# Kernel optimization log

Hardware: AMD Instinct MI355X
Metric: run time of the kernel (lower is better)

The kernel has to match this reference:

```python
import jax, jax.numpy as jnp
import numpy as np

EMB = 1024
HEADS = 16
EPS = 1e-6


def setup_inputs() -> dict:
    key = jax.random.key(0)
    ks = jax.random.split(key, 11)
    B, T = 4, 2048
    s = 0.02
    inp = {
        "x": jax.random.normal(ks[0], (B, T, EMB), dtype=jnp.float32),
        "Wq": jax.random.normal(ks[1], (EMB, EMB), dtype=jnp.float32) * s,
        "bq": jnp.zeros((EMB,), dtype=jnp.float32),
        "Wk": jax.random.normal(ks[2], (EMB, EMB), dtype=jnp.float32) * s,
        "bk": jnp.zeros((EMB,), dtype=jnp.float32),
        "Wv": jax.random.normal(ks[3], (EMB, EMB), dtype=jnp.float32) * s,
        "bv": jnp.zeros((EMB,), dtype=jnp.float32),
        "Wp": jax.random.normal(ks[4], (EMB, EMB), dtype=jnp.float32) * s,
        "bp": jnp.zeros((EMB,), dtype=jnp.float32),
        "gamma": jnp.ones((EMB,), dtype=jnp.float32),
        "beta": jnp.zeros((EMB,), dtype=jnp.float32),
    }
    return inp


def reference(x, Wq, bq, Wk, bk, Wv, bv, Wp, bp, gamma, beta):
    B, T, E = x.shape
    H = HEADS
    hd = E // H
    residual = x
    # torch Linear: y = x @ W.T + b
    q = (jnp.einsum('bte,fe->btf', x, Wq) + bq).reshape(B, T, H, hd).transpose(0, 2, 1, 3)
    k = (jnp.einsum('bte,fe->btf', x, Wk) + bk).reshape(B, T, H, hd).transpose(0, 2, 1, 3)
    v = (jnp.einsum('bte,fe->btf', x, Wv) + bv).reshape(B, T, H, hd).transpose(0, 2, 1, 3)
    # NOTE: original scales by 1/sqrt(T), not 1/sqrt(head_size)
    scale = 1.0 / jnp.sqrt(jnp.asarray(T, dtype=x.dtype))
    att = jnp.einsum('bhqd,bhkd->bhqk', q, k) * scale
    causal = jnp.tril(jnp.ones((T, T), dtype=bool))
    att = jnp.where(causal, att, -jnp.inf)
    att = jax.nn.softmax(att, axis=-1)
    out = jnp.einsum('bhqk,bhkd->bhqd', att, v)
    out = out.transpose(0, 2, 1, 3).reshape(B, T, E)
    # residual added BEFORE projection (as in original)
    out = jnp.einsum('bte,fe->btf', out + residual, Wp) + bp
    # LayerNorm(eps=1e-6)
    mu = jnp.mean(out, axis=-1, keepdims=True)
    var = jnp.mean(jnp.square(out - mu), axis=-1, keepdims=True)
    out = (out - mu) / jnp.sqrt(var + EPS) * gamma + beta
    return out
```

## Files before the change

### kernel.cpp

```cpp
#include <hip/hip_runtime.h>
#include <hip/hip_bf16.h>
#include <cstdint>
#include <cstdio>

#define EMB    1024
#define HEADS  16
#define HD     64
#define TSEQ   2048
#define NBATCH 4
#define BT     (NBATCH*TSEQ)
#define QKVN   3072
#define QKLD   2048

#define CSCALE (1.4426950408889634f * 0.022097086912079608f)

typedef __hip_bfloat16 bf16;
typedef __attribute__((ext_vector_type(8))) short short8;
typedef __attribute__((ext_vector_type(4))) short short4v;
typedef __attribute__((ext_vector_type(4))) float f32x4;

#define MFMA32(A,B,C) __builtin_amdgcn_mfma_f32_16x16x32_bf16(A,B,C,0,0,0)
#if __has_builtin(__builtin_amdgcn_mfma_f32_16x16x16_bf16)
#define MFMA16(A,B,C) __builtin_amdgcn_mfma_f32_16x16x16_bf16(A,B,C,0,0,0)
#else
#define MFMA16(A,B,C) __builtin_amdgcn_mfma_f32_16x16x16bf16_1k(A,B,C,0,0,0)
#endif

#if __has_builtin(__builtin_amdgcn_exp2f)
#define EXP2(x) __builtin_amdgcn_exp2f(x)
#else
#define EXP2(x) exp2f(x)
#endif

template<bool B> struct BoolC { static constexpr bool value = B; };

__device__ __forceinline__ void gload_lds16(const void* g, void* l) {
  __builtin_amdgcn_global_load_lds(
      (const __attribute__((address_space(1))) void*)g,
      (__attribute__((address_space(3))) void*)l,
      16, 0, 0);
}

__device__ __forceinline__ unsigned pkbf(float a, float b) {
  unsigned ua = __builtin_bit_cast(unsigned, a) + 0x8000u;
  unsigned ub = __builtin_bit_cast(unsigned, b) + 0x8000u;
  return __builtin_amdgcn_perm(ub, ua, 0x07060302u);
}

#define BARRIER() do { asm volatile("" ::: "memory"); \
                       __builtin_amdgcn_s_barrier(); \
                       asm volatile("" ::: "memory"); } while (0)
#define BAR_VM(N) do { asm volatile("s_waitcnt vmcnt(" #N ")" ::: "memory"); \
                       __builtin_amdgcn_s_barrier(); \
                       asm volatile("" ::: "memory"); } while (0)

__global__ void fused_cast(const float* __restrict__ x, const float* __restrict__ Wq,
                           const float* __restrict__ Wk, const float* __restrict__ Wv,
                           const float* __restrict__ Wp, const float* __restrict__ bq,
                           const float* __restrict__ bk, const float* __restrict__ bv,
                           bf16* __restrict__ xb, bf16* __restrict__ wqkv,
                           bf16* __restrict__ wpb, float* __restrict__ biasqkv) {
  const int blk = blockIdx.x;
  const int i = threadIdx.x * 4;
  if (blk >= 12288) {
    const int wsel = blk - 12288;
    const float* bsrc = wsel == 0 ? bq : (wsel == 1 ? bk : bv);
    float4 bv4 = *(const float4*)(bsrc + i);
    if (wsel == 0) { bv4.x *= CSCALE; bv4.y *= CSCALE; bv4.z *= CSCALE; bv4.w *= CSCALE; }
    *(float4*)(biasqkv + wsel * 1024 + i) = bv4;
    return;
  }
  const float* src; bf16* dst; float sc = 1.0f;
  if (blk < 8192)       { src = x  + (size_t)blk * 1024;           dst = xb   + (size_t)blk * 1024; }
  else if (blk < 9216)  { src = Wq + (size_t)(blk - 8192) * 1024;  dst = wqkv + (size_t)(blk - 8192) * 1024; sc = CSCALE; }
  else if (blk < 10240) { src = Wk + (size_t)(blk - 9216) * 1024;  dst = wqkv + ((size_t)1 << 20) + (size_t)(blk - 9216) * 1024; }
  else if (blk < 11264) { src = Wv + (size_t)(blk - 10240) * 1024; dst = wqkv + ((size_t)2 << 20) + (size_t)(blk - 10240) * 1024; }
  else                  { src = Wp + (size_t)(blk - 11264) * 1024; dst = wpb  + (size_t)(blk - 11264) * 1024; }
  float4 v = *(const float4*)(src + i);
  union { short4v v; bf16 b[4]; } u;
  u.b[0] = __float2bfloat16(v.x * sc); u.b[1] = __float2bfloat16(v.y * sc);
  u.b[2] = __float2bfloat16(v.z * sc); u.b[3] = __float2bfloat16(v.w * sc);
  *(short4v*)(dst + i) = u.v;
}

#define PHASE_MFMA(MI0, NJ0) do { \
  __builtin_amdgcn_s_setprio(1); \
  _Pragma("unroll") \
  for (int m2 = 0; m2 < 4; ++m2) { \
    _Pragma("unroll") \
    for (int n2 = 0; n2 < 2; ++n2) { \
      acc[(MI0)+m2][(NJ0)+n2] = MFMA32(af[m2][0], bfr[(NJ0)+n2][0], acc[(MI0)+m2][(NJ0)+n2]); \
      acc[(MI0)+m2][(NJ0)+n2] = MFMA32(af[m2][1], bfr[(NJ0)+n2][1], acc[(MI0)+m2][(NJ0)+n2]); \
    } \
  } \
  __builtin_amdgcn_s_setprio(0); \
} while (0)

#define TILE(T, P) { \
  const int kn = ((T) + 1) * 64; \
  const bool st = (T) < 15; \
  const char* aB = rdA + (P) * 32768; \
  const char* bB = rdB + (P) * 32768; \
  char* sA = ldsA + ((P) ^ 1) * 32768 + wbase; \
  char* sB = ldsB + ((P) ^ 1) * 32768 + wbase; \
   \
  _Pragma("unroll") \
  for (int m2 = 0; m2 < 4; ++m2) { \
    af[m2][0] = *(const short8*)(aB + m2 * 2048 + cs0); \
    af[m2][1] = *(const short8*)(aB + m2 * 2048 + cs1); \
  } \
  _Pragma("unroll") \
  for (int n2 = 0; n2 < 2; ++n2) { \
    bfr[n2][0] = *(const short8*)(bB + n2 * 2048 + cs0); \
    bfr[n2][1] = *(const short8*)(bB + n2 * 2048 + cs1); \
  } \
  if (st) { gload_lds16(gB + kn,          sB);         \
            gload_lds16(gB + 131072 + kn, sB + 16384); } \
  BARRIER(); \
  PHASE_MFMA(0, 0); \
  BARRIER(); \
   \
  _Pragma("unroll") \
  for (int n2 = 2; n2 < 4; ++n2) { \
    bfr[n2][0] = *(const short8*)(bB + n2 * 2048 + cs0); \
    bfr[n2][1] = *(const short8*)(bB + n2 * 2048 + cs1); \
  } \
  if (st) { gload_lds16(gA + kn,          sA);         \
            gload_lds16(gA + 131072 + kn, sA + 16384); } \
  BARRIER(); \
  PHASE_MFMA(0, 2); \
  if (st) { BAR_VM(4); } else { BAR_VM(0); } \
   \
  _Pragma("unroll") \
  for (int m2 = 0; m2 < 4; ++m2) { \
    af[m2][0] = *(const short8*)(aB + (4 + m2) * 2048 + cs0); \
    af[m2][1] = *(const short8*)(aB + (4 + m2) * 2048 + cs1); \
  } \
  if (st) { gload_lds16(gB + 65536 + kn,  sB + 8192);  \
            gload_lds16(gB + 196608 + kn, sB + 24576); } \
  BARRIER(); \
  PHASE_MFMA(4, 2); \
  BARRIER(); \
   \
  if (st) { gload_lds16(gA + 65536 + kn,  sA + 8192);  \
            gload_lds16(gA + 196608 + kn, sA + 24576); } \
  PHASE_MFMA(4, 0); \
  if (st) { BAR_VM(2); } \
}

__global__ __launch_bounds__(512, 2) void gemm_qkv8(
    const bf16* __restrict__ A, const bf16* __restrict__ B,
    const float* __restrict__ bias, bf16* __restrict__ qkout,
    bf16* __restrict__ vt) {
  __shared__ short smem[65536];
  const int tid = threadIdx.x;
  const int l = tid & 63, w = tid >> 6;
  const int r = l & 15, qd = l >> 4;
  const int wm = w >> 2, wn = w & 3;

  const int f0 = blockIdx.x;
  const int sid = (f0 & 7) * 48 + (f0 >> 3);
  const int m0 = (sid / 12) * 256;
  const int n0 = (sid % 12) * 256;

  const int rowA = tid >> 3;
  const int chk = (tid & 7) ^ (rowA & 7);
  const bf16* gA = A + (size_t)(m0 + rowA) * 1024 + chk * 8;
  const bf16* gB = B + (size_t)(n0 + rowA) * 1024 + chk * 8;
  char* ldsA = (char*)smem;
  char* ldsB = (char*)smem + 65536;
  const int wbase = w * 1024;

  const char* rdA = (const char*)smem + wm * 16384 + r * 128;
  const char* rdB = (const char*)smem + 65536 + (wn >> 1) * 16384 +
                    ((wn & 1) * 64 + r) * 128;
  const int cs0 = (qd ^ (r & 7)) * 16;
  const int cs1 = ((4 + qd) ^ (r & 7)) * 16;

  f32x4 acc[8][4];
#pragma unroll
  for (int i = 0; i < 8; ++i)
#pragma unroll
    for (int j = 0; j < 4; ++j) acc[i][j] = (f32x4){0.f, 0.f, 0.f, 0.f};
  short8 af[4][2], bfr[4][2];

  {
    char* sA = ldsA + wbase;
    char* sB = ldsB + wbase;
    gload_lds16(gB,          sB);
    gload_lds16(gB + 131072, sB + 16384);
    gload_lds16(gA,          sA);
    gload_lds16(gA + 131072, sA + 16384);
    gload_lds16(gB + 65536,  sB + 8192);
    gload_lds16(gB + 196608, sB + 24576);
    gload_lds16(gA + 65536,  sA + 8192);
    gload_lds16(gA + 196608, sA + 24576);
    BAR_VM(2);
  }

#pragma unroll 1
  for (int tt = 0; tt < 8; ++tt) {
    TILE(tt * 2, 0)
    TILE(tt * 2 + 1, 1)
  }

  if (n0 < 2048) {
#pragma unroll
    for (int nt = 0; nt < 4; ++nt) {
      const int col = n0 + wn * 64 + nt * 16 + r;
      const float bv = bias[col];
#pragma unroll
      for (int mi = 0; mi < 8; ++mi) {
#pragma unroll
        for (int reg = 0; reg < 4; ++reg) {
          const int row = m0 + wm * 128 + mi * 16 + qd * 4 + reg;
          qkout[(size_t)row * QKLD + col] = __float2bfloat16(acc[mi][nt][reg] + bv);
        }
      }
    }
  } else {
    char* img = (char*)smem;
#pragma unroll
    for (int nt = 0; nt < 4; ++nt) {
      const int c_local = wn * 64 + nt * 16 + r;
      const float bv = bias[n0 + c_local];
      const int d7 = c_local & 7;
#pragma unroll
      for (int mi = 0; mi < 8; ++mi) {
        const int tbase = wm * 128 + mi * 16 + qd * 4;
        const int chunk = tbase >> 6;
        const int sbits = ((tbase >> 3) ^ d7) & 7;
        union { short4v v; bf16 b[4]; } u;
#pragma unroll
        for (int reg = 0; reg < 4; ++reg)
          u.b[reg] = __float2bfloat16(acc[mi][nt][reg] + bv);
        *(short4v*)(img + c_local * 512 + chunk * 128 + sbits * 16 + (qd & 1) * 8) = u.v;
      }
    }
    __syncthreads();
    const int bb = m0 >> 11, tb = m0 & 2047;
    const int hb = (n0 - 2048) >> 6;
    const int off = (tid & 31) * 16;
#pragma unroll
    for (int i = 0; i < 16; ++i) {
      const int row = i * 16 + (tid >> 5);
      const int h2 = hb + (row >> 6), d = row & 63;
      const f32x4 vv = *(const f32x4*)(img + row * 512 + off);
      char* dst = (char*)(vt + ((size_t)(bb * 16 + h2) * 64 + d) * 2048 + tb) + off;
      *(f32x4*)dst = vv;
    }
  }
}

template<int MODE>
__global__ __launch_bounds__(256) void gemm_bt(
    const bf16* __restrict__ A, const bf16* __restrict__ B,
    const float* __restrict__ bias, void* __restrict__ out0,
    bf16* __restrict__ vt, int M, int N, int K) {
  __shared__ bf16 As[128 * 32];
  __shared__ bf16 Bs[128 * 32];
  const int tid = threadIdx.x;
  const int l = tid & 63, w = tid >> 6;
  const int r = l & 15, q = l >> 4;
  const int m0 = blockIdx.y * 128, n0 = blockIdx.x * 128;
  const int wm = w >> 1, wn = w & 1;

  f32x4 acc[4][4];
#pragma unroll
  for (int i = 0; i < 4; ++i)
#pragma unroll
    for (int j = 0; j < 4; ++j) acc[i][j] = (f32x4){0.f, 0.f, 0.f, 0.f};

  const int slot0 = w * 64 + l;
  const int rowS0 = slot0 >> 2, chS0 = (slot0 & 3) * 8;
  const int slot1 = 256 + slot0;
  const int rowS1 = slot1 >> 2, chS1 = (slot1 & 3) * 8;

  const bf16* A0 = A + (size_t)(m0 + rowS0) * K + chS0;
  const bf16* A1 = A + (size_t)(m0 + rowS1) * K + chS1;
  const bf16* B0 = B + (size_t)(n0 + rowS0) * K + chS0;
  const bf16* B1 = B + (size_t)(n0 + rowS1) * K + chS1;
  char* AsD0 = (char*)As + w * 1024;
  char* AsD1 = (char*)As + 4096 + w * 1024;
  char* BsD0 = (char*)Bs + w * 1024;
  char* BsD1 = (char*)Bs + 4096 + w * 1024;

  for (int k0 = 0; k0 < K; k0 += 32) {
    __syncthreads();
    gload_lds16(A0 + k0, AsD0);
    gload_lds16(A1 + k0, AsD1);
    gload_lds16(B0 + k0, BsD0);
    gload_lds16(B1 + k0, BsD1);
    __syncthreads();

    short8 af[4], bfr[4];
#pragma unroll
    for (int mt = 0; mt < 4; ++mt)
      af[mt] = *(const short8*)(As + (wm * 64 + mt * 16 + r) * 32 + q * 8);
#pragma unroll
    for (int nt = 0; nt < 4; ++nt)
      bfr[nt] = *(const short8*)(Bs + (wn * 64 + nt * 16 + r) * 32 + q * 8);
#pragma unroll
    for (int mt = 0; mt < 4; ++mt)
#pragma unroll
      for (int nt = 0; nt < 4; ++nt)
        acc[mt][nt] = MFMA32(af[mt], bfr[nt], acc[mt][nt]);
  }

#pragma unroll
  for (int nt = 0; nt < 4; ++nt) {
    const int col = n0 + wn * 64 + nt * 16 + r;
    const float bv = bias[col];
#pragma unroll
    for (int mt = 0; mt < 4; ++mt) {
#pragma unroll
      for (int reg = 0; reg < 4; ++reg) {
        const int row = m0 + wm * 64 + mt * 16 + q * 4 + reg;
        const float v = acc[mt][nt][reg] + bv;
        if (MODE == 1) {
          ((float*)out0)[(size_t)row * N + col] = v;
        } else if (n0 < 2048) {
          ((bf16*)out0)[(size_t)row * QKLD + col] = __float2bfloat16(v);
        } else {
          const int f = col - 2048, h = f >> 6, d = f & 63;
          const int b = row >> 11, t = row & 2047;
          const int swz = (t & ~63) | ((((t >> 3) ^ d) & 7) << 3) | (t & 7);
          vt[((size_t)(b * 16 + h) * 64 + d) * 2048 + swz] = __float2bfloat16(v);
        }
      }
    }
  }
}

__global__ __launch_bounds__(256, 2) void flash7(
    const bf16* __restrict__ qk, const bf16* __restrict__ vt,
    const float* __restrict__ x, bf16* __restrict__ pb) {
  const int bh = blockIdx.x;
  const int ip = blockIdx.y;
  const int b = bh >> 4, h = bh & 15;
  const int qt[4] = { 31 - ip, 23 - ip, ip + 8, ip };
  const int tid = threadIdx.x, l = tid & 63, w = tid >> 6;
  const int r = l & 15, quad = l >> 4;

  __shared__ bf16 VtL[2][64 * 64];

  const bf16* Qbase = qk + (size_t)b * TSEQ * QKLD + h * HD;
  const bf16* Kbase = Qbase + 1024;
  const bf16* Vhead = vt + (size_t)bh * 64 * 2048;

  const int sl0 = tid, sl1 = 256 + tid;
  const bf16* vg0 = Vhead + (size_t)(sl0 >> 3) * 2048 + (sl0 & 7) * 8;
  const bf16* vg1 = Vhead + (size_t)(sl1 >> 3) * 2048 + (sl1 & 7) * 8;
  char* ldsb0[2] = { (char*)&VtL[0][0] + w * 1024, (char*)&VtL[1][0] + w * 1024 };
  char* ldsb1[2] = { (char*)&VtL[0][0] + 4096 + w * 1024, (char*)&VtL[1][0] + 4096 + w * 1024 };

  short8 qf0[4], qf1[4];
#pragma unroll
  for (int t = 0; t < 4; ++t) {
    const bf16* qp = Qbase + (size_t)(qt[t] * 64 + w * 16 + r) * QKLD + quad * 8;
    qf0[t] = *(const short8*)qp;
    qf1[t] = *(const short8*)(qp + 32);
  }

  f32x4 o[4][4], lac[4];
#pragma unroll
  for (int t = 0; t < 4; ++t) {
    lac[t] = (f32x4){0.f, 0.f, 0.f, 0.f};
#pragma unroll
    for (int nt = 0; nt < 4; ++nt) o[t][nt] = (f32x4){0.f, 0.f, 0.f, 0.f};
  }

  short4v ones4;
#pragma unroll
  for (int j = 0; j < 4; ++j) ones4[j] = (short)0x3F80;

  short4v vf[4][4];

  const bf16* Kl = Kbase + (size_t)r * QKLD + quad * 8;
  auto loadK = [&](int kt, short8 (&k0)[4], short8 (&k1)[4]) {
#pragma unroll
    for (int g = 0; g < 4; ++g) {
      const bf16* kp = Kl + (size_t)(kt * 64 + g * 16) * QKLD;
      k0[g] = *(const short8*)kp;
      k1[g] = *(const short8*)(kp + 32);
    }
  };

  short8 kA0[4], kA1[4], kB0[4], kB1[4];

  gload_lds16(vg0, ldsb0[0]);
  gload_lds16(vg1, ldsb1[0]);
  loadK(0, kA0, kA1);
  int bsel = 0;

  const int ktmax = qt[0];
  const int qrow_l = w * 16 + r;

  auto tilestep = [&](int t, auto diagc, short8 (&k0)[4], short8 (&k1)[4],
                      int kt) {
    constexpr bool D = decltype(diagc)::value;
    f32x4 s[4];
#pragma unroll
    for (int g = 0; g < 4; ++g) {
      f32x4 a = (f32x4){0.f, 0.f, 0.f, 0.f};
      a = MFMA32(k0[g], qf0[t], a);
      a = MFMA32(k1[g], qf1[t], a);
      s[g] = a;
    }
    short4v pA[4];
#pragma unroll
    for (int g = 0; g < 4; ++g) {
      float p[4];
#pragma unroll
      for (int reg = 0; reg < 4; ++reg) {
        float e = EXP2(s[g][reg]);
        if (D) {
          const int kj = g * 16 + quad * 4 + reg;
          if (kj > qrow_l) e = 0.f;
        }
        p[reg] = e;
      }
      union { short4v v; unsigned u[2]; } pu;
      pu.u[0] = pkbf(p[0], p[1]);
      pu.u[1] = pkbf(p[2], p[3]);
      pA[g] = pu.v;
    }
#pragma unroll
    for (int nt = 0; nt < 4; ++nt)
#pragma unroll
      for (int g = 0; g < 4; ++g)
        o[t][nt] = MFMA16(pA[g], vf[nt][g], o[t][nt]);
#pragma unroll
    for (int g = 0; g < 4; ++g)
      lac[t] = MFMA16(pA[g], ones4, lac[t]);
  };

  auto ktbody = [&](int kt, short8 (&kc0)[4], short8 (&kc1)[4],
                    short8 (&kn0)[4], short8 (&kn1)[4]) {
    __syncthreads();
    if (kt < ktmax) {
      gload_lds16(vg0 + (kt + 1) * 64, ldsb0[bsel ^ 1]);
      gload_lds16(vg1 + (kt + 1) * 64, ldsb1[bsel ^ 1]);
      loadK(kt + 1, kn0, kn1);
    }
    {
      const bf16* V = &VtL[bsel][0];
#pragma unroll
      for (int nt = 0; nt < 4; ++nt)
#pragma unroll
        for (int g = 0; g < 4; ++g)
          vf[nt][g] = *(const short4v*)(V + (nt * 16 + r) * 64 +
                                        (((g * 2 + (quad >> 1)) ^ (r & 7)) * 8) + (quad & 1) * 4);
    }
    if (kt == qt[0]) tilestep(0, BoolC<true>{}, kc0, kc1, kt);
    else             tilestep(0, BoolC<false>{}, kc0, kc1, kt);
    if (kt <= qt[1]) { if (kt == qt[1]) tilestep(1, BoolC<true>{}, kc0, kc1, kt);
                       else             tilestep(1, BoolC<false>{}, kc0, kc1, kt); }
    if (kt <= qt[2]) { if (kt == qt[2]) tilestep(2, BoolC<true>{}, kc0, kc1, kt);
                       else             tilestep(2, BoolC<false>{}, kc0, kc1, kt); }
    if (kt <= qt[3]) { if (kt == qt[3]) tilestep(3, BoolC<true>{}, kc0, kc1, kt);
                       else             tilestep(3, BoolC<false>{}, kc0, kc1, kt); }
    bsel ^= 1;
  };

  int kt = 0;
#pragma unroll 1
  for (; kt + 1 <= ktmax; kt += 2) {
    ktbody(kt,     kA0, kA1, kB0, kB1);
    ktbody(kt + 1, kB0, kB1, kA0, kA1);
  }
  if (kt <= ktmax) ktbody(kt, kA0, kA1, kB0, kB1);

#pragma unroll
  for (int t = 0; t < 4; ++t) {
#pragma unroll
    for (int reg = 0; reg < 4; ++reg) {
      const float inv = 1.0f / lac[t][reg];
      const int row = qt[t] * 64 + w * 16 + quad * 4 + reg;
      const float* xr = x + (size_t)(b * TSEQ + row) * EMB + h * HD;
      bf16* pr = pb + (size_t)(b * TSEQ + row) * EMB + h * HD;
#pragma unroll
      for (int nt = 0; nt < 4; ++nt) {
        const int d = nt * 16 + r;
        pr[d] = __float2bfloat16(o[t][nt][reg] * inv + xr[d]);
      }
    }
  }
}

__global__ __launch_bounds__(256) void ln_kernel(float* __restrict__ out,
                                                 const float* __restrict__ gamma,
                                                 const float* __restrict__ beta) {
  const int row = blockIdx.x;
  const int tid = threadIdx.x;
  float* p = out + (size_t)row * EMB;
  float4 v = ((const float4*)p)[tid];
  float s = v.x + v.y + v.z + v.w;
  float ss = v.x * v.x + v.y * v.y + v.z * v.z + v.w * v.w;
#pragma unroll
  for (int m = 1; m < 64; m <<= 1) {
    s += __shfl_xor(s, m, 64);
    ss += __shfl_xor(ss, m, 64);
  }
  __shared__ float red[8];
  const int w = tid >> 6, l = tid & 63;
  if (l == 0) { red[w] = s; red[4 + w] = ss; }
  __syncthreads();
  s = red[0] + red[1] + red[2] + red[3];
  ss = red[4] + red[5] + red[6] + red[7];
  const float mu = s * (1.0f / EMB);
  const float var = ss * (1.0f / EMB) - mu * mu;
  const float rs = rsqrtf(var + 1e-6f);
  const float4 g = ((const float4*)gamma)[tid];
  const float4 bb = ((const float4*)beta)[tid];
  float4 o;
  o.x = (v.x - mu) * rs * g.x + bb.x;
  o.y = (v.y - mu) * rs * g.y + bb.y;
  o.z = (v.z - mu) * rs * g.z + bb.z;
  o.w = (v.w - mu) * rs * g.w + bb.w;
  ((float4*)p)[tid] = o;
}

extern "C" void kernel_launch(void* const* d_in, const int* in_sizes, int n_in,
                              void* d_out, int out_size, void* d_ws, size_t ws_size,
                              hipStream_t stream) {
  const float* x     = (const float*)d_in[0];
  const float* Wq    = (const float*)d_in[1];
  const float* bq    = (const float*)d_in[2];
  const float* Wk    = (const float*)d_in[3];
  const float* bk    = (const float*)d_in[4];
  const float* Wv    = (const float*)d_in[5];
  const float* bv    = (const float*)d_in[6];
  const float* Wp    = (const float*)d_in[7];
  const float* bp    = (const float*)d_in[8];
  const float* gamma = (const float*)d_in[9];
  const float* beta  = (const float*)d_in[10];
  float* out = (float*)d_out;

  if (ws_size < (size_t)74 * 1024 * 1024) {
    printf("kernel_launch: ws_size %zu too small\n", ws_size);
    return;
  }
  char* ws = (char*)d_ws;
  bf16* xb    = (bf16*)ws;
  bf16* wqkv  = (bf16*)(ws + ((size_t)16 << 20));
  bf16* wpb   = (bf16*)(ws + ((size_t)22 << 20));
  float* bqkv = (float*)(ws + ((size_t)24 << 20));
  bf16* qkbuf = (bf16*)(ws + ((size_t)25 << 20));
  bf16* vtbuf = (bf16*)(ws + ((size_t)57 << 20));
  bf16* pbuf  = xb;

  fused_cast<<<12291, 256, 0, stream>>>(x, Wq, Wk, Wv, Wp, bq, bk, bv, xb, wqkv, wpb, bqkv);

  gemm_qkv8<<<dim3(384), dim3(512), 0, stream>>>(xb, wqkv, bqkv, qkbuf, vtbuf);

  flash7<<<dim3(64, 8), 256, 0, stream>>>(qkbuf, vtbuf, x, pbuf);

  gemm_bt<1><<<dim3(8, 64), 256, 0, stream>>>(pbuf, wpb, bp, out, nullptr, BT, EMB, EMB);

  ln_kernel<<<BT, 256, 0, stream>>>(out, gamma, beta);
}
```

Measured before the change: 285.9 us.

## Replace projection GEMM with pipelined 256x128 double-buffered kernel; add MFMA priority hints

The simple 128x128 projection GEMM, which synchronised twice per 32-wide K step, is replaced by a 512-thread 256x128 tile kernel. The new kernel uses 64-wide K steps, double-buffered swizzled LDS, staggered global-to-LDS loads interleaved with MFMA phases, and block-index remapping for L2 locality. It also raises wave priority around the MFMA sections in both the projection kernel and the flash attention tile step, so matrix ops get issued ahead of other waves. The new kernel is hardcoded to M=8192, N=K=1024 and uses 96KB of LDS, which limits occupancy.

```diff
diff --git a/kernel.cpp b/kernel.cpp
--- a/kernel.cpp
+++ b/kernel.cpp
@@ -252,81 +252,136 @@
   }
 }
 
-template<int MODE>
-__global__ __launch_bounds__(256) void gemm_bt(
+#define PJ_MFMA(MI0) do { \
+  __builtin_amdgcn_s_setprio(1); \
+  _Pragma("unroll") \
+  for (int m2 = 0; m2 < 2; ++m2) { \
+    _Pragma("unroll") \
+    for (int nj = 0; nj < 2; ++nj) { \
+      acc[(MI0)+m2][nj] = MFMA32(af[m2][0], bfr[nj][0], acc[(MI0)+m2][nj]); \
+      acc[(MI0)+m2][nj] = MFMA32(af[m2][1], bfr[nj][1], acc[(MI0)+m2][nj]); \
+    } \
+  } \
+  __builtin_amdgcn_s_setprio(0); \
+} while (0)
+
+#define PJ_TILE(T, P) { \
+  const int kn = ((T) + 1) * 64; \
+  const bool st = (T) < 15; \
+  const char* aB = rdA + (P) * 32768; \
+  const char* bB = rdB + (P) * 16384; \
+  char* sA = ldsA + ((P) ^ 1) * 32768 + wbase; \
+  char* sB = ldsB + ((P) ^ 1) * 16384 + wbase; \
+   \
+  _Pragma("unroll") \
+  for (int m2 = 0; m2 < 2; ++m2) { \
+    af[m2][0] = *(const short8*)(aB + m2 * 2048 + cs0); \
+    af[m2][1] = *(const short8*)(aB + m2 * 2048 + cs1); \
+  } \
+  _Pragma("unroll") \
+  for (int nj = 0; nj < 2; ++nj) { \
+    bfr[nj][0] = *(const short8*)(bB + nj * 2048 + cs0); \
+    bfr[nj][1] = *(const short8*)(bB + nj * 2048 + cs1); \
+  } \
+  if (st) { gload_lds16(gB + kn,         sB); \
+            gload_lds16(gB + 65536 + kn, sB + 8192); } \
+  BARRIER(); \
+  PJ_MFMA(0); \
+  BARRIER(); \
+   \
+  _Pragma("unroll") \
+  for (int m2 = 0; m2 < 2; ++m2) { \
+    af[m2][0] = *(const short8*)(aB + (2 + m2) * 2048 + cs0); \
+    af[m2][1] = *(const short8*)(aB + (2 + m2) * 2048 + cs1); \
+  } \
+  if (st) { gload_lds16(gA + kn,          sA); \
+            gload_lds16(gA + 131072 + kn, sA + 16384); } \
+  BARRIER(); \
+  PJ_MFMA(2); \
+  if (st) { BAR_VM(4); } else { BAR_VM(0); } \
+   \
+  _Pragma("unroll") \
+  for (int m2 = 0; m2 < 2; ++m2) { \
+    af[m2][0] = *(const short8*)(aB + (4 + m2) * 2048 + cs0); \
+    af[m2][1] = *(const short8*)(aB + (4 + m2) * 2048 + cs1); \
+  } \
+  if (st) { gload_lds16(gA + 65536 + kn,  sA + 8192); \
+            gload_lds16(gA + 196608 + kn, sA + 24576); } \
+  BARRIER(); \
+  PJ_MFMA(4); \
+  BARRIER(); \
+   \
+  _Pragma("unroll") \
+  for (int m2 = 0; m2 < 2; ++m2) { \
+    af[m2][0] = *(const short8*)(aB + (6 + m2) * 2048 + cs0); \
+    af[m2][1] = *(const short8*)(aB + (6 + m2) * 2048 + cs1); \
+  } \
+  PJ_MFMA(6); \
+  if (st) { BAR_VM(2); } \
+}
+
+__global__ __launch_bounds__(512, 2) void gemm_proj8(
     const bf16* __restrict__ A, const bf16* __restrict__ B,
-    const float* __restrict__ bias, void* __restrict__ out0,
-    bf16* __restrict__ vt, int M, int N, int K) {
-  __shared__ bf16 As[128 * 32];
-  __shared__ bf16 Bs[128 * 32];
+    const float* __restrict__ bias, float* __restrict__ out) {
+  __shared__ short smem[49152];
   const int tid = threadIdx.x;
   const int l = tid & 63, w = tid >> 6;
-  const int r = l & 15, q = l >> 4;
-  const int m0 = blockIdx.y * 128, n0 = blockIdx.x * 128;
-  const int wm = w >> 1, wn = w & 1;
-
-  f32x4 acc[4][4];
-#pragma unroll
-  for (int i = 0; i < 4; ++i)
-#pragma unroll
-    for (int j = 0; j < 4; ++j) acc[i][j] = (f32x4){0.f, 0.f, 0.f, 0.f};
-
-  const int slot0 = w * 64 + l;
-  const int rowS0 = slot0 >> 2, chS0 = (slot0 & 3) * 8;
-  const int slot1 = 256 + slot0;
-  const int rowS1 = slot1 >> 2, chS1 = (slot1 & 3) * 8;
-
-  const bf16* A0 = A + (size_t)(m0 + rowS0) * K + chS0;
-  const bf16* A1 = A + (size_t)(m0 + rowS1) * K + chS1;
-  const bf16* B0 = B + (size_t)(n0 + rowS0) * K + chS0;
-  const bf16* B1 = B + (size_t)(n0 + rowS1) * K + chS1;
-  char* AsD0 = (char*)As + w * 1024;
-  char* AsD1 = (char*)As + 4096 + w * 1024;
-  char* BsD0 = (char*)Bs + w * 1024;
-  char* BsD1 = (char*)Bs + 4096 + w * 1024;
-
-  for (int k0 = 0; k0 < K; k0 += 32) {
-    __syncthreads();
-    gload_lds16(A0 + k0, AsD0);
-    gload_lds16(A1 + k0, AsD1);
-    gload_lds16(B0 + k0, BsD0);
-    gload_lds16(B1 + k0, BsD1);
-    __syncthreads();
-
-    short8 af[4], bfr[4];
-#pragma unroll
-    for (int mt = 0; mt < 4; ++mt)
-      af[mt] = *(const short8*)(As + (wm * 64 + mt * 16 + r) * 32 + q * 8);
-#pragma unroll
-    for (int nt = 0; nt < 4; ++nt)
-      bfr[nt] = *(const short8*)(Bs + (wn * 64 + nt * 16 + r) * 32 + q * 8);
-#pragma unroll
-    for (int mt = 0; mt < 4; ++mt)
-#pragma unroll
-      for (int nt = 0; nt < 4; ++nt)
-        acc[mt][nt] = MFMA32(af[mt], bfr[nt], acc[mt][nt]);
-  }
-
-#pragma unroll
-  for (int nt = 0; nt < 4; ++nt) {
-    const int col = n0 + wn * 64 + nt * 16 + r;
+  const int r = l & 15, qd = l >> 4;
+  const int wm = w >> 2, wn = w & 3;
+
+  const int f0 = blockIdx.x;
+  const int sid = (f0 & 7) * 32 + (f0 >> 3);
+  const int m0 = (sid >> 3) * 256;
+  const int n0 = (sid & 7) * 128;
+
+  const int rowA = tid >> 3;
+  const int chk = (tid & 7) ^ (rowA & 7);
+  const bf16* gA = A + (size_t)(m0 + rowA) * 1024 + chk * 8;
+  const bf16* gB = B + (size_t)(n0 + rowA) * 1024 + chk * 8;
+  char* ldsA = (char*)smem;
+  char* ldsB = (char*)smem + 65536;
+  const int wbase = w * 1024;
+
+  const char* rdA = (const char*)smem + wm * 16384 + r * 128;
+  const char* rdB = (const char*)smem + 65536 + (wn * 32 + r) * 128;
+  const int cs0 = (qd ^ (r & 7)) * 16;
+  const int cs1 = ((4 + qd) ^ (r & 7)) * 16;
+
+  f32x4 acc[8][2];
+#pragma unroll
+  for (int i = 0; i < 8; ++i)
+#pragma unroll
+    for (int j = 0; j < 2; ++j) acc[i][j] = (f32x4){0.f, 0.f, 0.f, 0.f};
+  short8 af[2][2], bfr[2][2];
+
+  {
+    char* sA = ldsA + wbase;
+    char* sB = ldsB + wbase;
+    gload_lds16(gB,          sB);
+    gload_lds16(gB + 65536,  sB + 8192);
+    gload_lds16(gA,          sA);
+    gload_lds16(gA + 131072, sA + 16384);
+    gload_lds16(gA + 65536,  sA + 8192);
+    gload_lds16(gA + 196608, sA + 24576);
+    BAR_VM(2);
+  }
+
+#pragma unroll 1
+  for (int tt = 0; tt < 8; ++tt) {
+    PJ_TILE(tt * 2, 0)
+    PJ_TILE(tt * 2 + 1, 1)
+  }
+
+#pragma unroll
+  for (int nj = 0; nj < 2; ++nj) {
+    const int col = n0 + wn * 32 + nj * 16 + r;
     const float bv = bias[col];
 #pragma unroll
-    for (int mt = 0; mt < 4; ++mt) {
+    for (int mi = 0; mi < 8; ++mi) {
 #pragma unroll
       for (int reg = 0; reg < 4; ++reg) {
-        const int row = m0 + wm * 64 + mt * 16 + q * 4 + reg;
-        const float v = acc[mt][nt][reg] + bv;
-        if (MODE == 1) {
-          ((float*)out0)[(size_t)row * N + col] = v;
-        } else if (n0 < 2048) {
-          ((bf16*)out0)[(size_t)row * QKLD + col] = __float2bfloat16(v);
-        } else {
-          const int f = col - 2048, h = f >> 6, d = f & 63;
-          const int b = row >> 11, t = row & 2047;
-          const int swz = (t & ~63) | ((((t >> 3) ^ d) & 7) << 3) | (t & 7);
-          vt[((size_t)(b * 16 + h) * 64 + d) * 2048 + swz] = __float2bfloat16(v);
-        }
+        const int row = m0 + wm * 128 + mi * 16 + qd * 4 + reg;
+        out[(size_t)row * 1024 + col] = acc[mi][nj][reg] + bv;
       }
     }
   }
@@ -400,6 +455,7 @@
                       int kt) {
     constexpr bool D = decltype(diagc)::value;
     f32x4 s[4];
+    __builtin_amdgcn_s_setprio(1);
 #pragma unroll
     for (int g = 0; g < 4; ++g) {
       f32x4 a = (f32x4){0.f, 0.f, 0.f, 0.f};
@@ -407,6 +463,7 @@
       a = MFMA32(k1[g], qf1[t], a);
       s[g] = a;
     }
+    __builtin_amdgcn_s_setprio(0);
     short4v pA[4];
 #pragma unroll
     for (int g = 0; g < 4; ++g) {
@@ -425,6 +482,7 @@
       pu.u[1] = pkbf(p[2], p[3]);
       pA[g] = pu.v;
     }
+    __builtin_amdgcn_s_setprio(1);
 #pragma unroll
     for (int nt = 0; nt < 4; ++nt)
 #pragma unroll
@@ -433,6 +491,7 @@
 #pragma unroll
     for (int g = 0; g < 4; ++g)
       lac[t] = MFMA16(pA[g], ones4, lac[t]);
+    __builtin_amdgcn_s_setprio(0);
   };
 
   auto ktbody = [&](int kt, short8 (&kc0)[4], short8 (&kc1)[4],
@@ -556,7 +615,7 @@
 
   flash7<<<dim3(64, 8), 256, 0, stream>>>(qkbuf, vtbuf, x, pbuf);
 
-  gemm_bt<1><<<dim3(8, 64), 256, 0, stream>>>(pbuf, wpb, bp, out, nullptr, BT, EMB, EMB);
+  gemm_proj8<<<dim3(256), dim3(512), 0, stream>>>(pbuf, wpb, bp, out);
 
   ln_kernel<<<BT, 256, 0, stream>>>(out, gamma, beta);
 }
```

Result: faster. 275.0 us (-3.8%).
